# Optimization experiments

Measured on AMD Instinct MI355X. Metric: run time of the kernel, lower is better.

The kernel has to match this reference:

```python
import jax, jax.numpy as jnp
import numpy as np

D = 512   # dense write dimension
M = 64    # number of experts
B = 16    # per-expert sparse code width
N = 8192  # tokens
K = 4     # experts per token (top-k)


def _normalize_U(U):
    # UnitColNormPadded(dim=1): each column of the (D+1, b) expert matrix
    # is rescaled to unit L2 norm along the padded (D+1) axis.
    nrm = jnp.sqrt(jnp.sum(U * U, axis=1, keepdims=True))
    return U / nrm


def setup_inputs() -> dict:
    key = jax.random.key(0)
    k1, k2, k3 = jax.random.split(key, 3)
    h_sparse = jax.random.normal(k1, (N, K, B), dtype=jnp.float32)
    topk_idxs = jax.random.randint(k2, (N, K), 0, M)
    U = jax.random.normal(k3, (M, D + 1, B), dtype=jnp.float32)
    return {"h_sparse": h_sparse, "topk_idxs": topk_idxs, "U": U}


def reference(h_sparse, topk_idxs, U):
    Un = _normalize_U(U)                      # (m, D+1, b)
    U_active = Un[topk_idxs][:, :, :D, :]     # gather -> (N, k, D, b)
    writes = jnp.einsum('nkdb,nkb->nd', U_active, h_sparse)   # (N, D)
    h_recon = jnp.einsum('nkdb,nd->nkb', U_active, writes)    # (N, k, b)
    h_target = jax.lax.stop_gradient(h_sparse)
    diff = h_recon - h_target
    writer_aux_loss = jnp.mean(diff * diff)
    return writes, writer_aux_loss
```

## Files before the change

kernel.cpp:

```cpp
#include <hip/hip_runtime.h>

#define DD 512
#define MM 64
#define BB 16
#define NN 8192
#define KK 4
#define DP1 513
#define CAP 1024
#define GPE 8
#define NPAIR (NN * KK)

#define CNT_B  0
#define BKT_B  256
#define U_B    135424
#define UT_B   1184000
#define WBF_B  2232576
#define PART_B 10621184
#define WS_NEED 44175616

typedef unsigned int uint;
typedef unsigned short ushort;
typedef __attribute__((ext_vector_type(8))) short short8;
typedef __attribute__((ext_vector_type(4))) float f32x4;

__device__ __forceinline__ ushort f2bf(float f) {
    uint u = __builtin_bit_cast(uint, f);
    uint r = (u + 0x7FFFu + ((u >> 16) & 1u)) >> 16;
    return (ushort)r;
}
__device__ __forceinline__ float bf2f(ushort s) {
    return __builtin_bit_cast(float, (uint)s << 16);
}

__global__ __launch_bounds__(256) void prep_kernel(
    const float* __restrict__ U, void* __restrict__ ws,
    float* __restrict__ loss_slot)
{
    const int m = blockIdx.x, t = threadIdx.x;
    const float* Um = U + (long)m * DP1 * BB;

    __shared__ float red[256];
    __shared__ float inv_s[BB];
    __shared__ ushort tr[BB][DD + 8];

    float a = 0.f;
    for (int i = t; i < DP1 * BB; i += 256) { float v = Um[i]; a += v * v; }
    red[t] = a;
    __syncthreads();
    if (t < BB) {
        float tot = 0.f;
        #pragma unroll
        for (int j = 0; j < 16; ++j) tot += red[t + 16 * j];
        inv_s[t] = rsqrtf(tot);
    }
    __syncthreads();

    ushort* ub = (ushort*)((char*)ws + U_B) + (long)m * DD * BB;
    ushort* ut = (ushort*)((char*)ws + UT_B) + (long)m * BB * DD;

    #pragma unroll
    for (int iter = 0; iter < 16; ++iter) {
        const int i = t + iter * 256;
        const int e0 = 2 * i;
        const int d = e0 >> 4, b0 = e0 & 15;
        const float2 v = *(const float2*)(Um + e0);
        const ushort bv0 = f2bf(v.x * inv_s[b0]);
        const ushort bv1 = f2bf(v.y * inv_s[b0 + 1]);
        *(uint*)(ub + e0) = (uint)bv0 | ((uint)bv1 << 16);
        tr[b0][d] = bv0;
        tr[b0 + 1][d] = bv1;
    }
    __syncthreads();

    {
        const int b = t >> 4, base = (t & 15) * 32;
        #pragma unroll
        for (int j = 0; j < 4; ++j) {
            const int doff = base + j * 8;
            uint4 val;
            val.x = (uint)tr[b][doff + 0] | ((uint)tr[b][doff + 1] << 16);
            val.y = (uint)tr[b][doff + 2] | ((uint)tr[b][doff + 3] << 16);
            val.z = (uint)tr[b][doff + 4] | ((uint)tr[b][doff + 5] << 16);
            val.w = (uint)tr[b][doff + 6] | ((uint)tr[b][doff + 7] << 16);
            *(uint4*)(ut + (long)b * DD + doff) = val;
        }
    }
    if (m == 0 && t == 0) *loss_slot = 0.f;
}

__global__ __launch_bounds__(256) void build_buckets(
    const int* __restrict__ topk, void* __restrict__ ws)
{
    int* cnt = (int*)ws;
    ushort* bkt = (ushort*)((char*)ws + BKT_B);
    __shared__ int lc[MM], lb[MM];
    const int t = threadIdx.x;
    if (t < MM) lc[t] = 0;
    __syncthreads();
    const int p = blockIdx.x * 256 + t;
    const int e = topk[p];
    const int my = atomicAdd(&lc[e], 1);
    __syncthreads();
    if (t < MM) lb[t] = atomicAdd(&cnt[t], lc[t]);
    __syncthreads();
    bkt[e * CAP + lb[e] + my] = (ushort)p;
}

__global__ __launch_bounds__(256) void pass_writes_mfma(
    const float* __restrict__ h_sparse, void* __restrict__ ws)
{
    const int e = blockIdx.x >> 3, g = blockIdx.x & 7;
    const int wave = threadIdx.x >> 6, lane = threadIdx.x & 63;
    const int quad = lane >> 4, l15 = lane & 15;

    const int* cnt = (const int*)ws;
    const ushort* bkt = (const ushort*)((const char*)ws + BKT_B);
    const ushort* Ue = (const ushort*)((const char*)ws + U_B) + (long)e * DD * BB;
    ushort* part = (ushort*)((char*)ws + PART_B);

    const int c  = cnt[e];
    const int lo = (c * g) >> 3;
    const int hi = (c * (g + 1)) >> 3;

    for (int base = lo + wave * 16; base < hi; base += 64) {
        const int pidx = base + l15;
        const bool valid = pidx < hi;
        const int id = valid ? (int)bkt[e * CAP + pidx] : 0;
        const int n = id >> 2, k = id & 3;

        short8 bfrag = (short8)0;
        if (quad < 2 && valid) {
            const float4* hp = (const float4*)(h_sparse + (long)id * BB + quad * 8);
            const float4 h0 = hp[0], h1 = hp[1];
            bfrag[0] = (short)f2bf(h0.x); bfrag[1] = (short)f2bf(h0.y);
            bfrag[2] = (short)f2bf(h0.z); bfrag[3] = (short)f2bf(h0.w);
            bfrag[4] = (short)f2bf(h1.x); bfrag[5] = (short)f2bf(h1.y);
            bfrag[6] = (short)f2bf(h1.z); bfrag[7] = (short)f2bf(h1.w);
        }
        ushort* prow = part + ((long)(k * NN + n) << 9);

        #pragma unroll 2
        for (int dt = 0; dt < 32; dt += 2) {
            short8 a0 = (short8)0, a1 = (short8)0;
            if (quad < 2) {
                a0 = *(const short8*)(Ue + ((long)(dt * 16 + l15) << 4) + quad * 8);
                a1 = *(const short8*)(Ue + ((long)((dt + 1) * 16 + l15) << 4) + quad * 8);
            }
            f32x4 z = {0.f, 0.f, 0.f, 0.f};
            f32x4 c0 = __builtin_amdgcn_mfma_f32_16x16x32_bf16(a0, bfrag, z, 0, 0, 0);
            f32x4 c1 = __builtin_amdgcn_mfma_f32_16x16x32_bf16(a1, bfrag, z, 0, 0, 0);

            uint p0x = (uint)f2bf(c0[0]) | ((uint)f2bf(c0[1]) << 16);
            uint p0y = (uint)f2bf(c0[2]) | ((uint)f2bf(c0[3]) << 16);
            uint p1x = (uint)f2bf(c1[0]) | ((uint)f2bf(c1[1]) << 16);
            uint p1y = (uint)f2bf(c1[2]) | ((uint)f2bf(c1[3]) << 16);
            uint q0x = __shfl_xor((int)p0x, 16, 64);
            uint q0y = __shfl_xor((int)p0y, 16, 64);
            uint q1x = __shfl_xor((int)p1x, 16, 64);
            uint q1y = __shfl_xor((int)p1y, 16, 64);

            if (valid) {
                uint4 st;
                int sdt;
                if ((quad & 1) == 0) {
                    st.x = p0x; st.y = p0y; st.z = q0x; st.w = q0y;
                    sdt = dt;
                } else {
                    st.x = q1x; st.y = q1y; st.z = p1x; st.w = p1y;
                    sdt = dt + 1;
                }
                const int srow = (quad & 2) ? 8 : 0;
                *(uint4*)(prow + sdt * 16 + srow) = st;
            }
        }
    }
}

__global__ __launch_bounds__(256) void reduce_w(
    void* __restrict__ ws, float* __restrict__ out)
{
    const uint4* part4 = (const uint4*)((const char*)ws + PART_B);
    uint4* wbf4 = (uint4*)((char*)ws + WBF_B);
    const int gsz = NN * DD / 8;
    const int gid = blockIdx.x * 256 + threadIdx.x;

    const uint4 v0 = part4[gid];
    const uint4 v1 = part4[(long)gsz + gid];
    const uint4 v2 = part4[2L * gsz + gid];
    const uint4 v3 = part4[3L * gsz + gid];

    float s[8];
    s[0] = bf2f((ushort)v0.x) + bf2f((ushort)v1.x) + bf2f((ushort)v2.x) + bf2f((ushort)v3.x);
    s[1] = bf2f((ushort)(v0.x >> 16)) + bf2f((ushort)(v1.x >> 16)) + bf2f((ushort)(v2.x >> 16)) + bf2f((ushort)(v3.x >> 16));
    s[2] = bf2f((ushort)v0.y) + bf2f((ushort)v1.y) + bf2f((ushort)v2.y) + bf2f((ushort)v3.y);
    s[3] = bf2f((ushort)(v0.y >> 16)) + bf2f((ushort)(v1.y >> 16)) + bf2f((ushort)(v2.y >> 16)) + bf2f((ushort)(v3.y >> 16));
    s[4] = bf2f((ushort)v0.z) + bf2f((ushort)v1.z) + bf2f((ushort)v2.z) + bf2f((ushort)v3.z);
    s[5] = bf2f((ushort)(v0.z >> 16)) + bf2f((ushort)(v1.z >> 16)) + bf2f((ushort)(v2.z >> 16)) + bf2f((ushort)(v3.z >> 16));
    s[6] = bf2f((ushort)v0.w) + bf2f((ushort)v1.w) + bf2f((ushort)v2.w) + bf2f((ushort)v3.w);
    s[7] = bf2f((ushort)(v0.w >> 16)) + bf2f((ushort)(v1.w >> 16)) + bf2f((ushort)(v2.w >> 16)) + bf2f((ushort)(v3.w >> 16));

    float4* out4 = (float4*)out;
    out4[(long)gid * 2 + 0] = make_float4(s[0], s[1], s[2], s[3]);
    out4[(long)gid * 2 + 1] = make_float4(s[4], s[5], s[6], s[7]);

    uint4 pk;
    pk.x = (uint)f2bf(s[0]) | ((uint)f2bf(s[1]) << 16);
    pk.y = (uint)f2bf(s[2]) | ((uint)f2bf(s[3]) << 16);
    pk.z = (uint)f2bf(s[4]) | ((uint)f2bf(s[5]) << 16);
    pk.w = (uint)f2bf(s[6]) | ((uint)f2bf(s[7]) << 16);
    wbf4[gid] = pk;
}

__global__ __launch_bounds__(256) void pass_recon_mfma(
    const float* __restrict__ h_sparse, void* __restrict__ ws,
    float* __restrict__ out)
{
    const int e = blockIdx.x >> 3, g = blockIdx.x & 7;
    const int wave = threadIdx.x >> 6, lane = threadIdx.x & 63;
    const int quad = lane >> 4, l15 = lane & 15;
    const int t = threadIdx.x;

    const int* cnt = (const int*)ws;
    const ushort* bkt = (const ushort*)((const char*)ws + BKT_B);
    const ushort* Ute = (const ushort*)((const char*)ws + UT_B) + (long)e * BB * DD;
    const ushort* wbf = (const ushort*)((const char*)ws + WBF_B);

    __shared__ float loss_blk;
    if (t == 0) loss_blk = 0.f;
    __syncthreads();

    const int c  = cnt[e];
    const int lo = (c * g) >> 3;
    const int hi = (c * (g + 1)) >> 3;

    float lsum = 0.f;

    for (int base = lo + wave * 16; base < hi; base += 64) {
        const int pidx = base + l15;
        const bool valid = pidx < hi;
        const int id = valid ? (int)bkt[e * CAP + pidx] : 0;
        const int n = id >> 2;
        const ushort* wrow = wbf + ((long)n << 9);

        f32x4 acc = {0.f, 0.f, 0.f, 0.f};

        #pragma unroll 4
        for (int kk = 0; kk < 16; ++kk) {
            const int doff = kk * 32 + quad * 8;
            const short8 afrag = *(const short8*)(wrow + doff);
            const short8 bfrag = *(const short8*)(Ute + (long)l15 * DD + doff);
            acc = __builtin_amdgcn_mfma_f32_16x16x32_bf16(afrag, bfrag, acc, 0, 0, 0);
        }

        #pragma unroll
        for (int r = 0; r < 4; ++r) {
            const int pr = base + quad * 4 + r;
            if (pr < hi) {
                const int id2 = (int)bkt[e * CAP + pr];
                const float h = h_sparse[(long)id2 * BB + l15];
                const float d = acc[r] - h;
                lsum += d * d;
            }
        }
    }

    #pragma unroll
    for (int off = 32; off > 0; off >>= 1) lsum += __shfl_xor(lsum, off, 64);
    if (lane == 0 && lsum != 0.f) atomicAdd(&loss_blk, lsum);
    __syncthreads();
    if (t == 0 && loss_blk != 0.f)
        atomicAdd(out + (long)NN * DD, loss_blk * (1.0f / ((float)NN * KK * BB)));
}

__global__ __launch_bounds__(256) void norm_kernel(
    const float* __restrict__ U, float* __restrict__ inv_norm,
    float* __restrict__ loss_slot)
{
    const int m = blockIdx.x;
    const int t = threadIdx.x;
    const float* Um = U + (long)m * DP1 * BB;
    float acc = 0.f;
    for (int idx = t; idx < DP1 * BB; idx += 256) {
        float v = Um[idx];
        acc += v * v;
    }
    __shared__ float s[256];
    s[t] = acc;
    __syncthreads();
    if (t < BB) {
        float tot = 0.f;
        #pragma unroll
        for (int j = 0; j < 16; ++j) tot += s[t + 16 * j];
        inv_norm[m * BB + t] = rsqrtf(tot);
    }
    if (m == 0 && t == 0) *loss_slot = 0.f;
}

__global__ __launch_bounds__(256) void dense_write_kernel(
    const float* __restrict__ h_sparse,
    const int*   __restrict__ topk,
    const float* __restrict__ U,
    const float* __restrict__ inv_norm,
    float* __restrict__ out)
{
    const int n = blockIdx.x;
    const int t = threadIdx.x;

    __shared__ float hs[KK * BB];
    __shared__ float ho[KK * BB];
    __shared__ float inv_s[KK * BB];
    __shared__ int   eidx[KK];
    __shared__ float w_s[DD];
    __shared__ float red[256];

    if (t < KK) eidx[t] = topk[n * KK + t];
    __syncthreads();
    if (t < KK * BB) {
        const int k = t / BB, b = t % BB;
        const float h  = h_sparse[(long)n * KK * BB + t];
        const float iv = inv_norm[eidx[k] * BB + b];
        ho[t]    = h;
        inv_s[t] = iv;
        hs[t]    = h * iv;
    }
    __syncthreads();

    #pragma unroll
    for (int dd = 0; dd < 2; ++dd) {
        const int d = t + dd * 256;
        float w = 0.f;
        #pragma unroll
        for (int k = 0; k < KK; ++k) {
            const float4* row = (const float4*)(U + ((long)eidx[k] * DP1 + d) * BB);
            #pragma unroll
            for (int q = 0; q < 4; ++q) {
                const float4 u4 = row[q];
                w += u4.x * hs[k * BB + 4 * q + 0];
                w += u4.y * hs[k * BB + 4 * q + 1];
                w += u4.z * hs[k * BB + 4 * q + 2];
                w += u4.w * hs[k * BB + 4 * q + 3];
            }
        }
        w_s[d] = w;
        out[(long)n * DD + d] = w;
    }
    __syncthreads();

    {
        const int pair = t & 63;
        const int k = pair >> 4, b = pair & 15;
        const int ch = t >> 6;
        const float* Ucol = U + (long)eidx[k] * DP1 * BB + b;
        float p = 0.f;
        #pragma unroll 8
        for (int d = ch * 128; d < ch * 128 + 128; ++d) {
            p += Ucol[(long)d * BB] * w_s[d];
        }
        red[t] = p;
    }
    __syncthreads();

    if (t < 64) {
        const float recon = (red[t] + red[t + 64] + red[t + 128] + red[t + 192]) * inv_s[t];
        const float diff  = recon - ho[t];
        float sq = diff * diff;
        #pragma unroll
        for (int off = 32; off > 0; off >>= 1) sq += __shfl_down(sq, off, 64);
        if (t == 0) {
            atomicAdd(out + (long)NN * DD, sq * (1.0f / ((float)NN * KK * BB)));
        }
    }
}


extern "C" void kernel_launch(void* const* d_in, const int* in_sizes, int n_in,
                              void* d_out, int out_size, void* d_ws, size_t ws_size,
                              hipStream_t stream) {
    const float* h_sparse = (const float*)d_in[0];
    const int*   topk     = (const int*)d_in[1];
    const float* U        = (const float*)d_in[2];
    float* out = (float*)d_out;

    if (ws_size >= (size_t)WS_NEED) {
        hipMemsetAsync(d_ws, 0, 256, stream);
        hipLaunchKernelGGL(prep_kernel, dim3(MM), dim3(256), 0, stream,
                           U, d_ws, out + (long)NN * DD);
        hipLaunchKernelGGL(build_buckets, dim3(NPAIR / 256), dim3(256), 0, stream,
                           topk, d_ws);
        hipLaunchKernelGGL(pass_writes_mfma, dim3(MM * GPE), dim3(256), 0, stream,
                           h_sparse, d_ws);
        hipLaunchKernelGGL(reduce_w, dim3(NN * DD / 8 / 256), dim3(256), 0, stream,
                           d_ws, out);
        hipLaunchKernelGGL(pass_recon_mfma, dim3(MM * GPE), dim3(256), 0, stream,
                           h_sparse, d_ws, out);
    } else {
        float* inv_norm = (float*)d_ws;
        hipLaunchKernelGGL(norm_kernel, dim3(MM), dim3(256), 0, stream,
                           U, inv_norm, out + (long)NN * DD);
        hipLaunchKernelGGL(dense_write_kernel, dim3(NN), dim3(256), 0, stream,
                           h_sparse, topk, U, inv_norm, out);
    }
}
```

Baseline: 127.2 us.

## Fuse the five-kernel pipeline into one cooperative kernel with grid syncs

Replaces the memset plus five separate launches with a single cooperative kernel of 512 blocks that runs every stage (normalize/transpose U, count, scan, bucket fill, writes MFMA, reduce, recon/loss) separated by grid.sync. Bucket building becomes deterministic, using per-block counts and an exclusive prefix scan instead of global atomics. U preparation is split across 4 blocks per expert. The aim is to remove launch gaps and the memset. The cost is grid-wide barriers and a fixed grid size that must fit co-resident, with the old multi-kernel path kept as a fallback.

```diff
diff --git a/kernel.cpp b/kernel.cpp
--- a/kernel.cpp
+++ b/kernel.cpp
@@ -1,4 +1,7 @@
 #include <hip/hip_runtime.h>
+#include <hip/hip_cooperative_groups.h>
+
+namespace cg = cooperative_groups;
 
 #define DD 512
 #define MM 64
@@ -7,16 +10,17 @@
 #define KK 4
 #define DP1 513
 #define CAP 1024
-#define GPE 8
 #define NPAIR (NN * KK)
+#define GRID_C 512
 
 #define CNT_B  0
-#define BKT_B  256
-#define U_B    135424
-#define UT_B   1184000
-#define WBF_B  2232576
-#define PART_B 10621184
-#define WS_NEED 44175616
+#define BLKC_B 256
+#define BKT_B  33024
+#define U_B    164096
+#define UT_B   1212672
+#define WBF_B  2261248
+#define PART_B 10649856
+#define WS_NEED 44204288
 
 typedef unsigned int uint;
 typedef unsigned short ushort;
@@ -32,13 +36,253 @@
     return __builtin_bit_cast(float, (uint)s << 16);
 }
 
+__global__ __launch_bounds__(256) void fused_all(
+    const float* __restrict__ h_sparse,
+    const int*   __restrict__ topk,
+    const float* __restrict__ U,
+    void* __restrict__ ws,
+    float* __restrict__ out)
+{
+    cg::grid_group grid = cg::this_grid();
+    const int blk = blockIdx.x, t = threadIdx.x;
+    const int wave = t >> 6, lane = t & 63;
+    const int quad = lane >> 4, l15 = lane & 15;
+
+    __shared__ float  s_red[256];
+    __shared__ float  s_inv[16];
+    __shared__ ushort s_tr[16][136];
+    __shared__ int    s_cnt[128];
+    __shared__ float  s_loss;
+
+    int*    cnt    = (int*)ws;
+    int*    blkc   = (int*)((char*)ws + BLKC_B);
+    ushort* bkt    = (ushort*)((char*)ws + BKT_B);
+    ushort* ubase  = (ushort*)((char*)ws + U_B);
+    ushort* utbase = (ushort*)((char*)ws + UT_B);
+    ushort* wbf    = (ushort*)((char*)ws + WBF_B);
+    ushort* part   = (ushort*)((char*)ws + PART_B);
+
+    if (blk < 256) {
+        const int m = blk >> 2, sl = blk & 3;
+        const float* Um = U + (long)m * DP1 * BB;
+        float a = 0.f;
+        for (int i = t; i < DP1 * BB; i += 256) { float v = Um[i]; a += v * v; }
+        s_red[t] = a;
+        __syncthreads();
+        if (t < 16) {
+            float tot = 0.f;
+            #pragma unroll
+            for (int j = 0; j < 16; ++j) tot += s_red[t + 16 * j];
+            s_inv[t] = rsqrtf(tot);
+        }
+        __syncthreads();
+        ushort* ub = ubase + (long)m * DD * BB;
+        ushort* ut = utbase + (long)m * BB * DD;
+        const float* Us = Um + sl * 2048;
+        #pragma unroll
+        for (int iter = 0; iter < 4; ++iter) {
+            const int i = t + iter * 256;
+            const int e0 = 2 * i;
+            const int dl = e0 >> 4, b0 = e0 & 15;
+            const float2 v = *(const float2*)(Us + e0);
+            const ushort bv0 = f2bf(v.x * s_inv[b0]);
+            const ushort bv1 = f2bf(v.y * s_inv[b0 + 1]);
+            *(uint*)(ub + sl * 2048 + e0) = (uint)bv0 | ((uint)bv1 << 16);
+            s_tr[b0][dl]     = bv0;
+            s_tr[b0 + 1][dl] = bv1;
+        }
+        __syncthreads();
+        {
+            const int b = t >> 4, doff = (t & 15) * 8;
+            uint4 val;
+            val.x = (uint)s_tr[b][doff + 0] | ((uint)s_tr[b][doff + 1] << 16);
+            val.y = (uint)s_tr[b][doff + 2] | ((uint)s_tr[b][doff + 3] << 16);
+            val.z = (uint)s_tr[b][doff + 4] | ((uint)s_tr[b][doff + 5] << 16);
+            val.w = (uint)s_tr[b][doff + 6] | ((uint)s_tr[b][doff + 7] << 16);
+            *(uint4*)(ut + (long)b * DD + sl * 128 + doff) = val;
+        }
+    } else if (blk < 384) {
+        const int cblk = blk - 256;
+        if (t < 64) s_cnt[t] = 0;
+        __syncthreads();
+        const int e = topk[cblk * 256 + t];
+        atomicAdd(&s_cnt[e], 1);
+        __syncthreads();
+        if (t < 64) blkc[cblk * 64 + t] = s_cnt[t];
+    } else if (blk == 384 && t == 0) {
+        out[(long)NN * DD] = 0.f;
+    }
+    grid.sync();
+
+    if (blk < 64) {
+        const int e = blk;
+        int orig = 0;
+        if (t < 128) { orig = blkc[t * 64 + e]; s_cnt[t] = orig; }
+        __syncthreads();
+        #pragma unroll
+        for (int off = 1; off < 128; off <<= 1) {
+            int add = (t < 128 && t >= off) ? s_cnt[t - off] : 0;
+            __syncthreads();
+            if (t < 128) s_cnt[t] += add;
+            __syncthreads();
+        }
+        if (t < 128) blkc[t * 64 + e] = s_cnt[t] - orig;
+        if (t == 127) cnt[e] = s_cnt[127];
+    }
+    grid.sync();
+
+    if (blk >= 256 && blk < 384) {
+        const int cblk = blk - 256;
+        if (t < 64) s_cnt[t] = 0;
+        __syncthreads();
+        const int p = cblk * 256 + t;
+        const int e = topk[p];
+        const int r = atomicAdd(&s_cnt[e], 1);
+        bkt[e * CAP + blkc[cblk * 64 + e] + r] = (ushort)p;
+    }
+    grid.sync();
+
+    {
+        const int e = blk & 63, g = blk >> 6;
+        const ushort* Ue = ubase + (long)e * DD * BB;
+        const int c  = cnt[e];
+        const int lo = (c * g) >> 3;
+        const int hi = (c * (g + 1)) >> 3;
+
+        for (int base2 = lo + wave * 16; base2 < hi; base2 += 64) {
+            const int pidx = base2 + l15;
+            const bool valid = pidx < hi;
+            const int id = valid ? (int)bkt[e * CAP + pidx] : 0;
+            const int n = id >> 2, k = id & 3;
+
+            short8 bfrag = (short8)0;
+            if (quad < 2 && valid) {
+                const float4* hp = (const float4*)(h_sparse + (long)id * BB + quad * 8);
+                const float4 h0 = hp[0], h1 = hp[1];
+                bfrag[0] = (short)f2bf(h0.x); bfrag[1] = (short)f2bf(h0.y);
+                bfrag[2] = (short)f2bf(h0.z); bfrag[3] = (short)f2bf(h0.w);
+                bfrag[4] = (short)f2bf(h1.x); bfrag[5] = (short)f2bf(h1.y);
+                bfrag[6] = (short)f2bf(h1.z); bfrag[7] = (short)f2bf(h1.w);
+            }
+            ushort* prow = part + ((long)(k * NN + n) << 9);
+
+            #pragma unroll 2
+            for (int dt = 0; dt < 32; dt += 2) {
+                short8 a0 = (short8)0, a1 = (short8)0;
+                if (quad < 2) {
+                    a0 = *(const short8*)(Ue + ((long)(dt * 16 + l15) << 4) + quad * 8);
+                    a1 = *(const short8*)(Ue + ((long)((dt + 1) * 16 + l15) << 4) + quad * 8);
+                }
+                f32x4 z = {0.f, 0.f, 0.f, 0.f};
+                f32x4 c0 = __builtin_amdgcn_mfma_f32_16x16x32_bf16(a0, bfrag, z, 0, 0, 0);
+                f32x4 c1 = __builtin_amdgcn_mfma_f32_16x16x32_bf16(a1, bfrag, z, 0, 0, 0);
+
+                uint p0x = (uint)f2bf(c0[0]) | ((uint)f2bf(c0[1]) << 16);
+                uint p0y = (uint)f2bf(c0[2]) | ((uint)f2bf(c0[3]) << 16);
+                uint p1x = (uint)f2bf(c1[0]) | ((uint)f2bf(c1[1]) << 16);
+                uint p1y = (uint)f2bf(c1[2]) | ((uint)f2bf(c1[3]) << 16);
+                uint q0x = __shfl_xor((int)p0x, 16, 64);
+                uint q0y = __shfl_xor((int)p0y, 16, 64);
+                uint q1x = __shfl_xor((int)p1x, 16, 64);
+                uint q1y = __shfl_xor((int)p1y, 16, 64);
+
+                if (valid) {
+                    uint4 st;
+                    int sdt;
+                    if ((quad & 1) == 0) { st.x = p0x; st.y = p0y; st.z = q0x; st.w = q0y; sdt = dt; }
+                    else                 { st.x = q1x; st.y = q1y; st.z = p1x; st.w = p1y; sdt = dt + 1; }
+                    const int srow = (quad & 2) ? 8 : 0;
+                    *(uint4*)(prow + sdt * 16 + srow) = st;
+                }
+            }
+        }
+    }
+    grid.sync();
+
+    {
+        const uint4* part4 = (const uint4*)part;
+        uint4* wbf4 = (uint4*)wbf;
+        float4* out4 = (float4*)out;
+        const int gsz = NN * DD / 8;
+        #pragma unroll
+        for (int j = 0; j < 4; ++j) {
+            const int gid = blk * 1024 + j * 256 + t;
+            const uint4 v0 = part4[gid];
+            const uint4 v1 = part4[(long)gsz + gid];
+            const uint4 v2 = part4[2L * gsz + gid];
+            const uint4 v3 = part4[3L * gsz + gid];
+            float s[8];
+            s[0] = bf2f((ushort)v0.x) + bf2f((ushort)v1.x) + bf2f((ushort)v2.x) + bf2f((ushort)v3.x);
+            s[1] = bf2f((ushort)(v0.x >> 16)) + bf2f((ushort)(v1.x >> 16)) + bf2f((ushort)(v2.x >> 16)) + bf2f((ushort)(v3.x >> 16));
+            s[2] = bf2f((ushort)v0.y) + bf2f((ushort)v1.y) + bf2f((ushort)v2.y) + bf2f((ushort)v3.y);
+            s[3] = bf2f((ushort)(v0.y >> 16)) + bf2f((ushort)(v1.y >> 16)) + bf2f((ushort)(v2.y >> 16)) + bf2f((ushort)(v3.y >> 16));
+            s[4] = bf2f((ushort)v0.z) + bf2f((ushort)v1.z) + bf2f((ushort)v2.z) + bf2f((ushort)v3.z);
+            s[5] = bf2f((ushort)(v0.z >> 16)) + bf2f((ushort)(v1.z >> 16)) + bf2f((ushort)(v2.z >> 16)) + bf2f((ushort)(v3.z >> 16));
+            s[6] = bf2f((ushort)v0.w) + bf2f((ushort)v1.w) + bf2f((ushort)v2.w) + bf2f((ushort)v3.w);
+            s[7] = bf2f((ushort)(v0.w >> 16)) + bf2f((ushort)(v1.w >> 16)) + bf2f((ushort)(v2.w >> 16)) + bf2f((ushort)(v3.w >> 16));
+            out4[(long)gid * 2 + 0] = make_float4(s[0], s[1], s[2], s[3]);
+            out4[(long)gid * 2 + 1] = make_float4(s[4], s[5], s[6], s[7]);
+            uint4 pk;
+            pk.x = (uint)f2bf(s[0]) | ((uint)f2bf(s[1]) << 16);
+            pk.y = (uint)f2bf(s[2]) | ((uint)f2bf(s[3]) << 16);
+            pk.z = (uint)f2bf(s[4]) | ((uint)f2bf(s[5]) << 16);
+            pk.w = (uint)f2bf(s[6]) | ((uint)f2bf(s[7]) << 16);
+            wbf4[gid] = pk;
+        }
+    }
+    grid.sync();
+
+    {
+        if (t == 0) s_loss = 0.f;
+        __syncthreads();
+        const int e = blk & 63, g = blk >> 6;
+        const ushort* Ute = utbase + (long)e * BB * DD;
+        const int c  = cnt[e];
+        const int lo = (c * g) >> 3;
+        const int hi = (c * (g + 1)) >> 3;
+
+        float lsum = 0.f;
+        for (int base2 = lo + wave * 16; base2 < hi; base2 += 64) {
+            const int pidx = base2 + l15;
+            const bool valid = pidx < hi;
+            const int id = valid ? (int)bkt[e * CAP + pidx] : 0;
+            const int n = id >> 2;
+            const ushort* wrow = wbf + ((long)n << 9);
+
+            f32x4 acc = {0.f, 0.f, 0.f, 0.f};
+            #pragma unroll 4
+            for (int kk = 0; kk < 16; ++kk) {
+                const int doff = kk * 32 + quad * 8;
+                const short8 afrag = *(const short8*)(wrow + doff);
+                const short8 bfrag = *(const short8*)(Ute + (long)l15 * DD + doff);
+                acc = __builtin_amdgcn_mfma_f32_16x16x32_bf16(afrag, bfrag, acc, 0, 0, 0);
+            }
+            #pragma unroll
+            for (int r = 0; r < 4; ++r) {
+                const int pr = base2 + quad * 4 + r;
+                if (pr < hi) {
+                    const int id2 = (int)bkt[e * CAP + pr];
+                    const float h = h_sparse[(long)id2 * BB + l15];
+                    const float d = acc[r] - h;
+                    lsum += d * d;
+                }
+            }
+        }
+        #pragma unroll
+        for (int off = 32; off > 0; off >>= 1) lsum += __shfl_xor(lsum, off, 64);
+        if (lane == 0 && lsum != 0.f) atomicAdd(&s_loss, lsum);
+        __syncthreads();
+        if (t == 0 && s_loss != 0.f)
+            atomicAdd(out + (long)NN * DD, s_loss * (1.0f / ((float)NN * KK * BB)));
+    }
+}
+
 __global__ __launch_bounds__(256) void prep_kernel(
     const float* __restrict__ U, void* __restrict__ ws,
     float* __restrict__ loss_slot)
 {
     const int m = blockIdx.x, t = threadIdx.x;
     const float* Um = U + (long)m * DP1 * BB;
-
     __shared__ float red[256];
     __shared__ float inv_s[BB];
     __shared__ ushort tr[BB][DD + 8];
@@ -71,7 +315,6 @@
         tr[b0 + 1][d] = bv1;
     }
     __syncthreads();
-
     {
         const int b = t >> 4, base = (t & 15) * 32;
         #pragma unroll
@@ -85,7 +328,10 @@
             *(uint4*)(ut + (long)b * DD + doff) = val;
         }
     }
-    if (m == 0 && t == 0) *loss_slot = 0.f;
+    if (m == 0) {
+        if (t == 0) *loss_slot = 0.f;
+        if (t < 64) ((int*)ws)[t] = 0;
+    }
 }
 
 __global__ __launch_bounds__(256) void build_buckets(
@@ -109,7 +355,7 @@
 __global__ __launch_bounds__(256) void pass_writes_mfma(
     const float* __restrict__ h_sparse, void* __restrict__ ws)
 {
-    const int e = blockIdx.x >> 3, g = blockIdx.x & 7;
+    const int e = blockIdx.x & 63, g = blockIdx.x >> 6;
     const int wave = threadIdx.x >> 6, lane = threadIdx.x & 63;
     const int quad = lane >> 4, l15 = lane & 15;
 
@@ -162,13 +408,8 @@
             if (valid) {
                 uint4 st;
                 int sdt;
-                if ((quad & 1) == 0) {
-                    st.x = p0x; st.y = p0y; st.z = q0x; st.w = q0y;
-                    sdt = dt;
-                } else {
-                    st.x = q1x; st.y = q1y; st.z = p1x; st.w = p1y;
-                    sdt = dt + 1;
-                }
+                if ((quad & 1) == 0) { st.x = p0x; st.y = p0y; st.z = q0x; st.w = q0y; sdt = dt; }
+                else                 { st.x = q1x; st.y = q1y; st.z = p1x; st.w = p1y; sdt = dt + 1; }
                 const int srow = (quad & 2) ? 8 : 0;
                 *(uint4*)(prow + sdt * 16 + srow) = st;
             }
@@ -215,7 +456,7 @@
     const float* __restrict__ h_sparse, void* __restrict__ ws,
     float* __restrict__ out)
 {
-    const int e = blockIdx.x >> 3, g = blockIdx.x & 7;
+    const int e = blockIdx.x & 63, g = blockIdx.x >> 6;
     const int wave = threadIdx.x >> 6, lane = threadIdx.x & 63;
     const int quad = lane >> 4, l15 = lane & 15;
     const int t = threadIdx.x;
@@ -234,7 +475,6 @@
     const int hi = (c * (g + 1)) >> 3;
 
     float lsum = 0.f;
-
     for (int base = lo + wave * 16; base < hi; base += 64) {
         const int pidx = base + l15;
         const bool valid = pidx < hi;
@@ -243,7 +483,6 @@
         const ushort* wrow = wbf + ((long)n << 9);
 
         f32x4 acc = {0.f, 0.f, 0.f, 0.f};
-
         #pragma unroll 4
         for (int kk = 0; kk < 16; ++kk) {
             const int doff = kk * 32 + quad * 8;
@@ -251,7 +490,6 @@
             const short8 bfrag = *(const short8*)(Ute + (long)l15 * DD + doff);
             acc = __builtin_amdgcn_mfma_f32_16x16x32_bf16(afrag, bfrag, acc, 0, 0, 0);
         }
-
         #pragma unroll
         for (int r = 0; r < 4; ++r) {
             const int pr = base + quad * 4 + r;
@@ -263,7 +501,6 @@
             }
         }
     }
-
     #pragma unroll
     for (int off = 32; off > 0; off >>= 1) lsum += __shfl_xor(lsum, off, 64);
     if (lane == 0 && lsum != 0.f) atomicAdd(&loss_blk, lsum);
@@ -380,19 +617,25 @@
     const int*   topk     = (const int*)d_in[1];
     const float* U        = (const float*)d_in[2];
     float* out = (float*)d_out;
+    void* ws = d_ws;
 
     if (ws_size >= (size_t)WS_NEED) {
-        hipMemsetAsync(d_ws, 0, 256, stream);
-        hipLaunchKernelGGL(prep_kernel, dim3(MM), dim3(256), 0, stream,
-                           U, d_ws, out + (long)NN * DD);
-        hipLaunchKernelGGL(build_buckets, dim3(NPAIR / 256), dim3(256), 0, stream,
-                           topk, d_ws);
-        hipLaunchKernelGGL(pass_writes_mfma, dim3(MM * GPE), dim3(256), 0, stream,
-                           h_sparse, d_ws);
-        hipLaunchKernelGGL(reduce_w, dim3(NN * DD / 8 / 256), dim3(256), 0, stream,
-                           d_ws, out);
-        hipLaunchKernelGGL(pass_recon_mfma, dim3(MM * GPE), dim3(256), 0, stream,
-                           h_sparse, d_ws, out);
+        void* params[5] = { (void*)&h_sparse, (void*)&topk, (void*)&U,
+                            (void*)&ws, (void*)&out };
+        hipError_t err = hipLaunchCooperativeKernel(
+            fused_all, dim3(GRID_C), dim3(256), params, 0, stream);
+        if (err != hipSuccess) {
+            hipLaunchKernelGGL(prep_kernel, dim3(MM), dim3(256), 0, stream,
+                               U, ws, out + (long)NN * DD);
+            hipLaunchKernelGGL(build_buckets, dim3(NPAIR / 256), dim3(256), 0, stream,
+                               topk, ws);
+            hipLaunchKernelGGL(pass_writes_mfma, dim3(MM * 8), dim3(256), 0, stream,
+                               h_sparse, ws);
+            hipLaunchKernelGGL(reduce_w, dim3(NN * DD / 8 / 256), dim3(256), 0, stream,
+                               ws, out);
+            hipLaunchKernelGGL(pass_recon_mfma, dim3(MM * 8), dim3(256), 0, stream,
+                               h_sparse, ws, out);
+        }
     } else {
         float* inv_norm = (float*)d_ws;
         hipLaunchKernelGGL(norm_kernel, dim3(MM), dim3(256), 0, stream,
```

After: 419.7 us. 230% more time.

## Fuse U prep with bucket build and spread expert blocks across grid

Applied to the files above, without the earlier changes.

Merges the U normalisation/bf16 conversion kernel and the token-bucketing kernel into one launch. The U prep is split into four blocks per expert, each handling a quarter of the rows, so more CUs work on it. Blocks in the writes and recon passes are remapped so consecutive block ids hit different experts, which is meant to balance load across CUs. The cost is that each prep block recomputes the full column norms, so U is read redundantly, and the workspace offsets are shifted.

```diff
diff --git a/kernel.cpp b/kernel.cpp
--- a/kernel.cpp
+++ b/kernel.cpp
@@ -7,16 +7,15 @@
 #define KK 4
 #define DP1 513
 #define CAP 1024
-#define GPE 8
 #define NPAIR (NN * KK)
 
 #define CNT_B  0
-#define BKT_B  256
-#define U_B    135424
-#define UT_B   1184000
-#define WBF_B  2232576
-#define PART_B 10621184
-#define WS_NEED 44175616
+#define BKT_B  33024
+#define U_B    164096
+#define UT_B   1212672
+#define WBF_B  2261248
+#define PART_B 10649856
+#define WS_NEED 44204288
 
 typedef unsigned int uint;
 typedef unsigned short ushort;
@@ -32,51 +31,53 @@
     return __builtin_bit_cast(float, (uint)s << 16);
 }
 
-__global__ __launch_bounds__(256) void prep_kernel(
-    const float* __restrict__ U, void* __restrict__ ws,
+__global__ __launch_bounds__(256) void prep_build(
+    const float* __restrict__ U,
+    const int*   __restrict__ topk,
+    void* __restrict__ ws,
     float* __restrict__ loss_slot)
 {
-    const int m = blockIdx.x, t = threadIdx.x;
-    const float* Um = U + (long)m * DP1 * BB;
-
-    __shared__ float red[256];
-    __shared__ float inv_s[BB];
-    __shared__ ushort tr[BB][DD + 8];
-
-    float a = 0.f;
-    for (int i = t; i < DP1 * BB; i += 256) { float v = Um[i]; a += v * v; }
-    red[t] = a;
-    __syncthreads();
-    if (t < BB) {
-        float tot = 0.f;
-        #pragma unroll
-        for (int j = 0; j < 16; ++j) tot += red[t + 16 * j];
-        inv_s[t] = rsqrtf(tot);
-    }
-    __syncthreads();
-
-    ushort* ub = (ushort*)((char*)ws + U_B) + (long)m * DD * BB;
-    ushort* ut = (ushort*)((char*)ws + UT_B) + (long)m * BB * DD;
-
-    #pragma unroll
-    for (int iter = 0; iter < 16; ++iter) {
-        const int i = t + iter * 256;
-        const int e0 = 2 * i;
-        const int d = e0 >> 4, b0 = e0 & 15;
-        const float2 v = *(const float2*)(Um + e0);
-        const ushort bv0 = f2bf(v.x * inv_s[b0]);
-        const ushort bv1 = f2bf(v.y * inv_s[b0 + 1]);
-        *(uint*)(ub + e0) = (uint)bv0 | ((uint)bv1 << 16);
-        tr[b0][d] = bv0;
-        tr[b0 + 1][d] = bv1;
-    }
-    __syncthreads();
-
-    {
-        const int b = t >> 4, base = (t & 15) * 32;
-        #pragma unroll
-        for (int j = 0; j < 4; ++j) {
-            const int doff = base + j * 8;
+    const int blk = blockIdx.x, t = threadIdx.x;
+
+    if (blk < 256) {
+        const int m = blk >> 2, sl = blk & 3;
+        const float* Um = U + (long)m * DP1 * BB;
+
+        __shared__ float red[256];
+        __shared__ float inv_s[BB];
+        __shared__ ushort tr[BB][136];
+
+        float a = 0.f;
+        for (int i = t; i < DP1 * BB; i += 256) { float v = Um[i]; a += v * v; }
+        red[t] = a;
+        __syncthreads();
+        if (t < BB) {
+            float tot = 0.f;
+            #pragma unroll
+            for (int j = 0; j < 16; ++j) tot += red[t + 16 * j];
+            inv_s[t] = rsqrtf(tot);
+        }
+        __syncthreads();
+
+        ushort* ub = (ushort*)((char*)ws + U_B) + (long)m * DD * BB + sl * 2048;
+        ushort* ut = (ushort*)((char*)ws + UT_B) + (long)m * BB * DD + sl * 128;
+        const float* Us = Um + sl * 2048;
+
+        #pragma unroll
+        for (int iter = 0; iter < 4; ++iter) {
+            const int i = t + iter * 256;
+            const int e0 = 2 * i;
+            const int dl = e0 >> 4, b0 = e0 & 15;
+            const float2 v = *(const float2*)(Us + e0);
+            const ushort bv0 = f2bf(v.x * inv_s[b0]);
+            const ushort bv1 = f2bf(v.y * inv_s[b0 + 1]);
+            *(uint*)(ub + e0) = (uint)bv0 | ((uint)bv1 << 16);
+            tr[b0][dl]     = bv0;
+            tr[b0 + 1][dl] = bv1;
+        }
+        __syncthreads();
+        {
+            const int b = t >> 4, doff = (t & 15) * 8;
             uint4 val;
             val.x = (uint)tr[b][doff + 0] | ((uint)tr[b][doff + 1] << 16);
             val.y = (uint)tr[b][doff + 2] | ((uint)tr[b][doff + 3] << 16);
@@ -84,32 +85,28 @@
             val.w = (uint)tr[b][doff + 6] | ((uint)tr[b][doff + 7] << 16);
             *(uint4*)(ut + (long)b * DD + doff) = val;
         }
-    }
-    if (m == 0 && t == 0) *loss_slot = 0.f;
-}
-
-__global__ __launch_bounds__(256) void build_buckets(
-    const int* __restrict__ topk, void* __restrict__ ws)
-{
-    int* cnt = (int*)ws;
-    ushort* bkt = (ushort*)((char*)ws + BKT_B);
-    __shared__ int lc[MM], lb[MM];
-    const int t = threadIdx.x;
-    if (t < MM) lc[t] = 0;
-    __syncthreads();
-    const int p = blockIdx.x * 256 + t;
-    const int e = topk[p];
-    const int my = atomicAdd(&lc[e], 1);
-    __syncthreads();
-    if (t < MM) lb[t] = atomicAdd(&cnt[t], lc[t]);
-    __syncthreads();
-    bkt[e * CAP + lb[e] + my] = (ushort)p;
+    } else {
+        const int cblk = blk - 256;
+        int* cnt = (int*)ws;
+        ushort* bkt = (ushort*)((char*)ws + BKT_B);
+        __shared__ int lc[MM], lb[MM];
+        if (t < MM) lc[t] = 0;
+        __syncthreads();
+        const int p = cblk * 256 + t;
+        const int e = topk[p];
+        const int my = atomicAdd(&lc[e], 1);
+        __syncthreads();
+        if (t < MM) lb[t] = atomicAdd(&cnt[t], lc[t]);
+        __syncthreads();
+        bkt[e * CAP + lb[e] + my] = (ushort)p;
+        if (cblk == 0 && t == 0) *loss_slot = 0.f;
+    }
 }
 
 __global__ __launch_bounds__(256) void pass_writes_mfma(
     const float* __restrict__ h_sparse, void* __restrict__ ws)
 {
-    const int e = blockIdx.x >> 3, g = blockIdx.x & 7;
+    const int e = blockIdx.x & 63, g = blockIdx.x >> 6;
     const int wave = threadIdx.x >> 6, lane = threadIdx.x & 63;
     const int quad = lane >> 4, l15 = lane & 15;
 
@@ -162,13 +159,8 @@
             if (valid) {
                 uint4 st;
                 int sdt;
-                if ((quad & 1) == 0) {
-                    st.x = p0x; st.y = p0y; st.z = q0x; st.w = q0y;
-                    sdt = dt;
-                } else {
-                    st.x = q1x; st.y = q1y; st.z = p1x; st.w = p1y;
-                    sdt = dt + 1;
-                }
+                if ((quad & 1) == 0) { st.x = p0x; st.y = p0y; st.z = q0x; st.w = q0y; sdt = dt; }
+                else                 { st.x = q1x; st.y = q1y; st.z = p1x; st.w = p1y; sdt = dt + 1; }
                 const int srow = (quad & 2) ? 8 : 0;
                 *(uint4*)(prow + sdt * 16 + srow) = st;
             }
@@ -215,7 +207,7 @@
     const float* __restrict__ h_sparse, void* __restrict__ ws,
     float* __restrict__ out)
 {
-    const int e = blockIdx.x >> 3, g = blockIdx.x & 7;
+    const int e = blockIdx.x & 63, g = blockIdx.x >> 6;
     const int wave = threadIdx.x >> 6, lane = threadIdx.x & 63;
     const int quad = lane >> 4, l15 = lane & 15;
     const int t = threadIdx.x;
@@ -234,7 +226,6 @@
     const int hi = (c * (g + 1)) >> 3;
 
     float lsum = 0.f;
-
     for (int base = lo + wave * 16; base < hi; base += 64) {
         const int pidx = base + l15;
         const bool valid = pidx < hi;
@@ -243,7 +234,6 @@
         const ushort* wrow = wbf + ((long)n << 9);
 
         f32x4 acc = {0.f, 0.f, 0.f, 0.f};
-
         #pragma unroll 4
         for (int kk = 0; kk < 16; ++kk) {
             const int doff = kk * 32 + quad * 8;
@@ -251,7 +241,6 @@
             const short8 bfrag = *(const short8*)(Ute + (long)l15 * DD + doff);
             acc = __builtin_amdgcn_mfma_f32_16x16x32_bf16(afrag, bfrag, acc, 0, 0, 0);
         }
-
         #pragma unroll
         for (int r = 0; r < 4; ++r) {
             const int pr = base + quad * 4 + r;
@@ -263,7 +252,6 @@
             }
         }
     }
-
     #pragma unroll
     for (int off = 32; off > 0; off >>= 1) lsum += __shfl_xor(lsum, off, 64);
     if (lane == 0 && lsum != 0.f) atomicAdd(&loss_blk, lsum);
@@ -383,15 +371,13 @@
 
     if (ws_size >= (size_t)WS_NEED) {
         hipMemsetAsync(d_ws, 0, 256, stream);
-        hipLaunchKernelGGL(prep_kernel, dim3(MM), dim3(256), 0, stream,
-                           U, d_ws, out + (long)NN * DD);
-        hipLaunchKernelGGL(build_buckets, dim3(NPAIR / 256), dim3(256), 0, stream,
-                           topk, d_ws);
-        hipLaunchKernelGGL(pass_writes_mfma, dim3(MM * GPE), dim3(256), 0, stream,
+        hipLaunchKernelGGL(prep_build, dim3(256 + NPAIR / 256), dim3(256), 0, stream,
+                           U, topk, d_ws, out + (long)NN * DD);
+        hipLaunchKernelGGL(pass_writes_mfma, dim3(MM * 8), dim3(256), 0, stream,
                            h_sparse, d_ws);
         hipLaunchKernelGGL(reduce_w, dim3(NN * DD / 8 / 256), dim3(256), 0, stream,
                            d_ws, out);
-        hipLaunchKernelGGL(pass_recon_mfma, dim3(MM * GPE), dim3(256), 0, stream,
+        hipLaunchKernelGGL(pass_recon_mfma, dim3(MM * 8), dim3(256), 0, stream,
                            h_sparse, d_ws, out);
     } else {
         float* inv_norm = (float*)d_ws;
```

After: 126.5 us. Within noise of the previous version (-0.5%).
